# Optimization experiments

Measured on AMD Instinct MI355X. Metric: run time of the kernel, lower is better.

The kernel has to match this reference:

```python
import jax, jax.numpy as jnp
import numpy as np

N_BASIS = 20
R_MAX = 3.5

# e3nn normalize2mom constant for silu: 1/sqrt(E[silu(z)^2]), z~N(0,1) (analytic quadrature)
_trapz = getattr(np, "trapezoid", np.trapz)
_z = np.linspace(-12.0, 12.0, 100001)
_phi = np.exp(-0.5 * _z**2) / np.sqrt(2.0 * np.pi)
_silu = _z / (1.0 + np.exp(-_z))
SILU_CST = float(1.0 / np.sqrt(_trapz(_silu**2 * _phi, _z)))  # ~1.679


def norm_silu(x):
    return SILU_CST * jax.nn.silu(x)


def spherical_harmonics_lmax3(pos):
    # component-normalized real spherical harmonics up to l=3, e3nn axis convention (y up)
    u = pos / jnp.linalg.norm(pos, axis=-1, keepdims=True)
    x, y, z = u[..., 0], u[..., 1], u[..., 2]
    x2, y2, z2 = x * x, y * y, z * z
    s3, s5, s15 = jnp.sqrt(3.0), jnp.sqrt(5.0), jnp.sqrt(15.0)
    s7, s105 = jnp.sqrt(7.0), jnp.sqrt(105.0)
    s35_8, s21_8 = jnp.sqrt(35.0 / 8.0), jnp.sqrt(21.0 / 8.0)
    sh = [
        jnp.ones_like(x),                                                   # l=0
        s3 * x, s3 * y, s3 * z,                                             # l=1
        s15 * x * z, s15 * x * y, s5 * (y2 - 0.5 * (x2 + z2)),
        s15 * y * z, 0.5 * s15 * (z2 - x2),                                 # l=2
        s35_8 * x * (3.0 * z2 - x2), s105 * x * y * z,
        s21_8 * x * (5.0 * y2 - 1.0), 0.5 * s7 * y * (5.0 * y2 - 3.0),
        s21_8 * z * (5.0 * y2 - 1.0), 0.5 * s105 * y * (z2 - x2),
        s35_8 * z * (z2 - 3.0 * x2),                                        # l=3
    ]
    return jnp.stack(sh, axis=-1)  # [E, 16]


def soft_one_hot_gaussian(d):
    # e3nn soft_one_hot_linspace(start=0, end=3.5, number=20, basis='gaussian', cutoff=True)
    values = jnp.linspace(0.0, R_MAX, N_BASIS + 2)[1:-1]
    step = R_MAX / (N_BASIS + 1)
    diff = (d[:, None] - values[None, :]) / step
    return jnp.exp(-diff * diff) / 1.12


def setup_inputs() -> dict:
    E, N = 2_000_000, 125_000
    key = jax.random.key(0)
    k = jax.random.split(key, 6)
    return {
        "pos": jax.random.normal(k[0], (E, 3), jnp.float32),
        "x_right": jax.random.normal(k[1], (E, 1), jnp.float32),
        "x_left": jax.random.normal(k[2], (N, 1), jnp.float32),
        "W1": jax.random.normal(k[3], (20, 30), jnp.float32),
        "W2": jax.random.normal(k[4], (30, 5), jnp.float32),
        "origin_index": jax.random.randint(k[5], (E,), 0, N),
    }


def reference(pos, x_right, x_left, W1, W2, origin_index):
    sh = spherical_harmonics_lmax3(pos)                 # [E, 16], component norm
    d = jnp.linalg.norm(pos, axis=-1)                   # [E]
    emb = soft_one_hot_gaussian(d)                      # [E, 20]
    # e3nn FullyConnectedNet([20, 30, 5], silu): x @ W / sqrt(fan_in), normalized act on hidden
    h = norm_silu(emb @ (W1 / jnp.sqrt(jnp.asarray(W1.shape[0], jnp.float32))))
    tp_weights = h @ (W2 / jnp.sqrt(jnp.asarray(W2.shape[0], jnp.float32)))  # [E, 5]
    # tp1: FullyConnectedTensorProduct('1x0e', sh, '5x0e'): only CG path is 0e(x)0e->0e
    # (single path -> path-normalization factor 1; Y_0 = 1 under component normalization)
    h_right = tp_weights * x_right * sh[:, :1]          # [E, 5]
    # tp2: FullTensorProduct('1x0e', '5x0e') -> '5x0e': plain scalar product per channel
    product = x_left[origin_index] * h_right            # [E, 5]
    return jnp.sum(product)
```

## Files before the change

kernel.cpp:

```cpp
#include <hip/hip_runtime.h>


#define TN    2048
#define DMAXF 5.0f
#define TPB   256
#define TILE  1024

__device__ __constant__ float kSiluCst = 1.6765581f;

__global__ __launch_bounds__(256) void build_lut_kernel(
    const float* __restrict__ W1, const float* __restrict__ W2,
    float* __restrict__ table)
{
    int t = blockIdx.x * 256 + threadIdx.x;
    int entry = t >> 5;
    int k = t & 31;
    int kk = (k < 30) ? k : 29;

    float d  = (float)entry * (DMAXF / (float)TN);
    float t6 = 6.0f * d;
    const float w1scale = 1.0f / (1.12f * sqrtf(20.0f));

    float a = 0.0f;
    #pragma unroll
    for (int j = 0; j < 20; ++j) {
        float df = t6 - (float)(j + 1);
        float e  = __expf(-df * df);
        a = fmaf(e * w1scale, W1[j * 30 + kk], a);
    }
    float s = a / (1.0f + __expf(-a));

    float w2s = 0.0f;
    #pragma unroll
    for (int c = 0; c < 5; ++c) w2s += W2[kk * 5 + c];

    float contrib = (k < 30) ? s * w2s * (kSiluCst / sqrtf(30.0f)) : 0.0f;

    #pragma unroll
    for (int m = 16; m > 0; m >>= 1) contrib += __shfl_xor(contrib, m, 32);

    if (k == 0 && entry < TN) table[entry] = contrib;
}

__global__ __launch_bounds__(TPB) void edge_sum_kernel(
    const float* __restrict__ pos, const float* __restrict__ xr,
    const float* __restrict__ xl, const int* __restrict__ oi,
    const float* __restrict__ table, double* __restrict__ partials, int E)
{
    __shared__ float lut[TN];
    __shared__ float lpos[3 * TILE];
    __shared__ double swv[TPB / 64];

    const int tid = threadIdx.x;
    const long tile0 = (long)blockIdx.x * TILE;

    {
        const float4* t4 = (const float4*)table;
        float4* l4 = (float4*)lut;
        l4[tid]       = t4[tid];
        l4[tid + TPB] = t4[tid + TPB];
    }
    {
        const long  gbase4 = (tile0 * 3) / 4;
        const long  lim4   = (3L * E) / 4;
        const float4* g4 = (const float4*)pos;
        float4* l4 = (float4*)lpos;
        #pragma unroll
        for (int i = 0; i < 3; ++i) {
            int li = tid + i * TPB;
            long gi = gbase4 + li;
            if (gi < lim4) l4[li] = g4[gi];
        }
        long tail = lim4 * 4 + tid;
        if (tail < 3L * E && tail >= tile0 * 3 && tail < tile0 * 3 + 3 * TILE)
            lpos[tail - tile0 * 3] = pos[tail];
    }
    __syncthreads();

    const float scale = (float)TN / DMAXF;
    const float umax  = (float)(TN - 1) - 1e-3f;

    const int rem = (int)min((long)TILE, (long)E - tile0);
    const int e0  = tid * 4;
    double acc = 0.0;

    if (e0 + 4 <= rem) {
        const float4* lp4 = (const float4*)lpos;
        float4 a = lp4[3 * tid + 0];
        float4 b = lp4[3 * tid + 1];
        float4 c = lp4[3 * tid + 2];
        float4 xv = ((const float4*)(xr + tile0))[tid];
        int4   ov = ((const int4*)(oi + tile0))[tid];

        float px[4] = {a.x, a.w, b.z, c.y};
        float py[4] = {a.y, b.x, b.w, c.z};
        float pz[4] = {a.z, b.y, c.x, c.w};
        float xrv[4] = {xv.x, xv.y, xv.z, xv.w};
        float xlv[4];
        xlv[0] = xl[ov.x]; xlv[1] = xl[ov.y]; xlv[2] = xl[ov.z]; xlv[3] = xl[ov.w];

        float fsum = 0.0f;
        #pragma unroll
        for (int j = 0; j < 4; ++j) {
            float d  = sqrtf(fmaf(px[j], px[j], fmaf(py[j], py[j], pz[j] * pz[j])));
            float u  = fminf(d * scale, umax);
            int   i0 = (int)u;
            float fr = u - (float)i0;
            float f  = fmaf(fr, lut[i0 + 1] - lut[i0], lut[i0]);
            fsum = fmaf(f * xrv[j], xlv[j], fsum);
        }
        acc = (double)fsum;
    } else if (e0 < rem) {
        float fsum = 0.0f;
        for (int j = 0; j < 4 && e0 + j < rem; ++j) {
            int le = e0 + j;
            float x = lpos[3 * le], y = lpos[3 * le + 1], z = lpos[3 * le + 2];
            float d  = sqrtf(fmaf(x, x, fmaf(y, y, z * z)));
            float u  = fminf(d * scale, umax);
            int   i0 = (int)u;
            float fr = u - (float)i0;
            float f  = fmaf(fr, lut[i0 + 1] - lut[i0], lut[i0]);
            long  ge = tile0 + le;
            fsum = fmaf(f * xr[ge], xl[oi[ge]], fsum);
        }
        acc = (double)fsum;
    }

    #pragma unroll
    for (int off = 32; off > 0; off >>= 1) acc += __shfl_down(acc, off);
    int lane = tid & 63, wv = tid >> 6;
    if (lane == 0) swv[wv] = acc;
    __syncthreads();
    if (tid == 0)
        partials[blockIdx.x] = (swv[0] + swv[1]) + (swv[2] + swv[3]);
}

__global__ __launch_bounds__(256) void final_reduce_kernel(
    const double* __restrict__ partials, int n, float* __restrict__ out)
{
    __shared__ double sm[256];
    double a = 0.0;
    for (int i = threadIdx.x; i < n; i += 256) a += partials[i];
    sm[threadIdx.x] = a;
    __syncthreads();
    #pragma unroll
    for (int s = 128; s > 0; s >>= 1) {
        if (threadIdx.x < (unsigned)s) sm[threadIdx.x] += sm[threadIdx.x + s];
        __syncthreads();
    }
    if (threadIdx.x == 0) out[0] = (float)sm[0];
}

extern "C" void kernel_launch(void* const* d_in, const int* in_sizes, int n_in,
                              void* d_out, int out_size, void* d_ws, size_t ws_size,
                              hipStream_t stream) {
    const float* pos = (const float*)d_in[0];
    const float* xr  = (const float*)d_in[1];
    const float* xl  = (const float*)d_in[2];
    const float* W1  = (const float*)d_in[3];
    const float* W2  = (const float*)d_in[4];
    const int*   oi  = (const int*)d_in[5];
    float* out = (float*)d_out;

    int E = in_sizes[1];
    int nblk = (E + TILE - 1) / TILE;

    float*  table    = (float*)d_ws;
    double* partials = (double*)((char*)d_ws + (size_t)TN * sizeof(float));

    hipLaunchKernelGGL(build_lut_kernel, dim3((TN * 32) / 256), dim3(256), 0, stream,
                       W1, W2, table);
    hipLaunchKernelGGL(edge_sum_kernel, dim3(nblk), dim3(TPB), 0, stream,
                       pos, xr, xl, oi, table, partials, E);
    hipLaunchKernelGGL(final_reduce_kernel, dim3(1), dim3(256), 0, stream,
                       partials, nblk, out);
}
```

Before: 28.86 us.

## Drop final reduce kernel via atomics, load pos directly, 8 edges per thread

Removes the third kernel launch by zeroing the output inside the LUT kernel and having each edge block atomically add its float partial sum. It also stops staging positions in shared memory and has each thread load its 8 edges' positions straight from global memory as float4s, doubling edges per thread and halving the block count. This cuts a launch and an LDS round trip, but float atomics make the summation order nondeterministic and lose the double-precision cross-block reduction. With E a multiple of 8, the unaligned-float4 concern does not arise because g0*3*4 bytes is 16-byte aligned.

New measurement: 28.03 us. 2.9% less time.

```diff
diff --git a/kernel.cpp b/kernel.cpp
--- a/kernel.cpp
+++ b/kernel.cpp
@@ -4,14 +4,17 @@
 #define TN    2048
 #define DMAXF 5.0f
 #define TPB   256
-#define TILE  1024
+#define EPT   8
+#define TILE  (TPB * EPT)
 
 __device__ __constant__ float kSiluCst = 1.6765581f;
 
 __global__ __launch_bounds__(256) void build_lut_kernel(
     const float* __restrict__ W1, const float* __restrict__ W2,
-    float* __restrict__ table)
+    float* __restrict__ table, float* __restrict__ out)
 {
+    if (blockIdx.x == 0 && threadIdx.x == 0) out[0] = 0.0f;
+
     int t = blockIdx.x * 256 + threadIdx.x;
     int entry = t >> 5;
     int k = t & 31;
@@ -45,14 +48,12 @@
 __global__ __launch_bounds__(TPB) void edge_sum_kernel(
     const float* __restrict__ pos, const float* __restrict__ xr,
     const float* __restrict__ xl, const int* __restrict__ oi,
-    const float* __restrict__ table, double* __restrict__ partials, int E)
+    const float* __restrict__ table, float* __restrict__ out, int E)
 {
     __shared__ float lut[TN];
-    __shared__ float lpos[3 * TILE];
     __shared__ double swv[TPB / 64];
 
     const int tid = threadIdx.x;
-    const long tile0 = (long)blockIdx.x * TILE;
 
     {
         const float4* t4 = (const float4*)table;
@@ -60,48 +61,37 @@
         l4[tid]       = t4[tid];
         l4[tid + TPB] = t4[tid + TPB];
     }
-    {
-        const long  gbase4 = (tile0 * 3) / 4;
-        const long  lim4   = (3L * E) / 4;
-        const float4* g4 = (const float4*)pos;
-        float4* l4 = (float4*)lpos;
-        #pragma unroll
-        for (int i = 0; i < 3; ++i) {
-            int li = tid + i * TPB;
-            long gi = gbase4 + li;
-            if (gi < lim4) l4[li] = g4[gi];
-        }
-        long tail = lim4 * 4 + tid;
-        if (tail < 3L * E && tail >= tile0 * 3 && tail < tile0 * 3 + 3 * TILE)
-            lpos[tail - tile0 * 3] = pos[tail];
-    }
     __syncthreads();
 
     const float scale = (float)TN / DMAXF;
     const float umax  = (float)(TN - 1) - 1e-3f;
 
-    const int rem = (int)min((long)TILE, (long)E - tile0);
-    const int e0  = tid * 4;
+    const long tile0 = (long)blockIdx.x * TILE;
+    const int  rem   = (int)min((long)TILE, (long)E - tile0);
+    const int  e0    = tid * EPT;
     double acc = 0.0;
 
-    if (e0 + 4 <= rem) {
-        const float4* lp4 = (const float4*)lpos;
-        float4 a = lp4[3 * tid + 0];
-        float4 b = lp4[3 * tid + 1];
-        float4 c = lp4[3 * tid + 2];
-        float4 xv = ((const float4*)(xr + tile0))[tid];
-        int4   ov = ((const int4*)(oi + tile0))[tid];
+    if (e0 + EPT <= rem) {
+        const long g0 = tile0 + e0;
+        const float4* p4 = (const float4*)(pos + g0 * 3);
+        float4 P0 = p4[0], P1 = p4[1], P2 = p4[2], P3 = p4[3], P4 = p4[4], P5 = p4[5];
+        const float4* x4 = (const float4*)(xr + g0);
+        float4 X0 = x4[0], X1 = x4[1];
+        const int4* o4 = (const int4*)(oi + g0);
+        int4 O0 = o4[0], O1 = o4[1];
 
-        float px[4] = {a.x, a.w, b.z, c.y};
-        float py[4] = {a.y, b.x, b.w, c.z};
-        float pz[4] = {a.z, b.y, c.x, c.w};
-        float xrv[4] = {xv.x, xv.y, xv.z, xv.w};
-        float xlv[4];
-        xlv[0] = xl[ov.x]; xlv[1] = xl[ov.y]; xlv[2] = xl[ov.z]; xlv[3] = xl[ov.w];
+        float xlv[EPT];
+        xlv[0] = xl[O0.x]; xlv[1] = xl[O0.y]; xlv[2] = xl[O0.z]; xlv[3] = xl[O0.w];
+        xlv[4] = xl[O1.x]; xlv[5] = xl[O1.y]; xlv[6] = xl[O1.z]; xlv[7] = xl[O1.w];
+
+        float px[EPT] = {P0.x, P0.w, P1.z, P2.y, P3.x, P3.w, P4.z, P5.y};
+        float py[EPT] = {P0.y, P1.x, P1.w, P2.z, P3.y, P4.x, P4.w, P5.z};
+        float pz[EPT] = {P0.z, P1.y, P2.x, P2.w, P3.z, P4.y, P5.x, P5.w};
+        float xrv[EPT] = {X0.x, X0.y, X0.z, X0.w, X1.x, X1.y, X1.z, X1.w};
 
         float fsum = 0.0f;
         #pragma unroll
-        for (int j = 0; j < 4; ++j) {
+        for (int j = 0; j < EPT; ++j) {
             float d  = sqrtf(fmaf(px[j], px[j], fmaf(py[j], py[j], pz[j] * pz[j])));
             float u  = fminf(d * scale, umax);
             int   i0 = (int)u;
@@ -112,15 +102,14 @@
         acc = (double)fsum;
     } else if (e0 < rem) {
         float fsum = 0.0f;
-        for (int j = 0; j < 4 && e0 + j < rem; ++j) {
-            int le = e0 + j;
-            float x = lpos[3 * le], y = lpos[3 * le + 1], z = lpos[3 * le + 2];
+        for (int j = 0; j < EPT && e0 + j < rem; ++j) {
+            long  ge = tile0 + e0 + j;
+            float x = pos[3 * ge], y = pos[3 * ge + 1], z = pos[3 * ge + 2];
             float d  = sqrtf(fmaf(x, x, fmaf(y, y, z * z)));
             float u  = fminf(d * scale, umax);
             int   i0 = (int)u;
             float fr = u - (float)i0;
             float f  = fmaf(fr, lut[i0 + 1] - lut[i0], lut[i0]);
-            long  ge = tile0 + le;
             fsum = fmaf(f * xr[ge], xl[oi[ge]], fsum);
         }
         acc = (double)fsum;
@@ -131,24 +120,10 @@
     int lane = tid & 63, wv = tid >> 6;
     if (lane == 0) swv[wv] = acc;
     __syncthreads();
-    if (tid == 0)
-        partials[blockIdx.x] = (swv[0] + swv[1]) + (swv[2] + swv[3]);
-}
-
-__global__ __launch_bounds__(256) void final_reduce_kernel(
-    const double* __restrict__ partials, int n, float* __restrict__ out)
-{
-    __shared__ double sm[256];
-    double a = 0.0;
-    for (int i = threadIdx.x; i < n; i += 256) a += partials[i];
-    sm[threadIdx.x] = a;
-    __syncthreads();
-    #pragma unroll
-    for (int s = 128; s > 0; s >>= 1) {
-        if (threadIdx.x < (unsigned)s) sm[threadIdx.x] += sm[threadIdx.x + s];
-        __syncthreads();
+    if (tid == 0) {
+        double bsum = (swv[0] + swv[1]) + (swv[2] + swv[3]);
+        atomicAdd(out, (float)bsum);
     }
-    if (threadIdx.x == 0) out[0] = (float)sm[0];
 }
 
 extern "C" void kernel_launch(void* const* d_in, const int* in_sizes, int n_in,
@@ -165,13 +140,10 @@
     int E = in_sizes[1];
     int nblk = (E + TILE - 1) / TILE;
 
-    float*  table    = (float*)d_ws;
-    double* partials = (double*)((char*)d_ws + (size_t)TN * sizeof(float));
+    float* table = (float*)d_ws;
 
     hipLaunchKernelGGL(build_lut_kernel, dim3((TN * 32) / 256), dim3(256), 0, stream,
-                       W1, W2, table);
+                       W1, W2, table, out);
     hipLaunchKernelGGL(edge_sum_kernel, dim3(nblk), dim3(TPB), 0, stream,
-                       pos, xr, xl, oi, table, partials, E);
-    hipLaunchKernelGGL(final_reduce_kernel, dim3(1), dim3(256), 0, stream,
-                       partials, nblk, out);
+                       pos, xr, xl, oi, table, out, E);
 }
```
